# Performance work log

Hardware: AMD Instinct MI355X
Metric: run time of the kernel (lower is better)

## Reference

```python
import jax, jax.numpy as jnp
import numpy as np


def setup_inputs() -> dict:
    key = jax.random.key(0)
    ks = jax.random.split(key, 6)
    B, T, U, D, K, V = 4, 256, 64, 512, 512, 1000
    return {
        "enc_state": jax.random.normal(ks[0], (B, T, D), dtype=jnp.float32),
        "dec_state": jax.random.normal(ks[1], (B, U, D), dtype=jnp.float32),
        "W1": jax.random.normal(ks[2], (K, 2 * D), dtype=jnp.float32) * (1.0 / np.sqrt(2 * D)),
        "b1": jax.random.normal(ks[3], (K,), dtype=jnp.float32) * 0.01,
        "W2": jax.random.normal(ks[4], (V, K), dtype=jnp.float32) * (1.0 / np.sqrt(K)),
        "b2": jax.random.normal(ks[5], (V,), dtype=jnp.float32) * 0.01,
    }


def reference(enc_state, dec_state, W1, b1, W2, b2):
    # JointNet: Linear(concat(enc_bc, dec_bc)) -> tanh -> Linear.
    # Linear over the concat [enc; dec] equals split-weight matmuls broadcast-summed,
    # so we never materialize the [B,T,U,2D] concat tensor (same math).
    D_enc = enc_state.shape[-1]
    W1e, W1d = W1[:, :D_enc], W1[:, D_enc:]
    he = jnp.einsum('btd,kd->btk', enc_state, W1e)  # [B,T,K]
    hd = jnp.einsum('bud,kd->buk', dec_state, W1d)  # [B,U,K]
    h = jnp.tanh(he[:, :, None, :] + hd[:, None, :, :] + b1)  # [B,T,U,K]
    return jnp.einsum('btuk,vk->btuv', h, W2) + b2  # [B,T,U,V]
```

## Files before the change

### kernel.cpp

```cpp
#include <hip/hip_runtime.h>


typedef __bf16 bf16x8 __attribute__((ext_vector_type(8)));
typedef float  f32x4  __attribute__((ext_vector_type(4)));

#define B_   4
#define T_   256
#define U_   64
#define D_   512
#define K_   512
#define V_   1000

__device__ __forceinline__ float tanh_fast(float x) {
    float e = __expf(2.0f * x);
    float r = __builtin_amdgcn_rcpf(e + 1.0f);
    return fmaf(-2.0f, r, 1.0f);
}

__global__ __launch_bounds__(256) void w2conv_kernel(const float* __restrict__ W2,
                                                     __bf16* __restrict__ W2b) {
    int idx = (blockIdx.x * 256 + threadIdx.x) * 8;
    const f32x4* p = (const f32x4*)(W2 + idx);
    f32x4 a = p[0], b = p[1];
    bf16x8 o;
#pragma unroll
    for (int j = 0; j < 4; ++j) { o[j] = (__bf16)a[j]; o[4 + j] = (__bf16)b[j]; }
    *(bf16x8*)(W2b + idx) = o;
}

__global__ __launch_bounds__(256) void stage1_kernel(const float* __restrict__ enc,
                                                     const float* __restrict__ dec,
                                                     const float* __restrict__ W1,
                                                     float* __restrict__ he,
                                                     float* __restrict__ hd) {
    const int ct = blockIdx.x;
    const int rt = blockIdx.y;
    const bool isDec = rt >= 16;
    const float* X = isDec ? (dec + (rt - 16) * 64 * D_) : (enc + rt * 64 * D_);
    const int   woff = isDec ? D_ : 0;
    float*      Y = isDec ? (hd + (rt - 16) * 64 * K_) : (he + rt * 64 * K_);
    const int   k0 = ct * 64;

    __shared__ __align__(16) __bf16 As[64][72];
    __shared__ __align__(16) __bf16 Bs[64][72];

    const int tid  = threadIdx.x;
    const int lane = tid & 63, w = tid >> 6;
    const int wm = (w >> 1) * 32, wn = (w & 1) * 32;
    const int q = lane >> 4, li = lane & 15;

    f32x4 acc[2][2] = {};

    for (int d0 = 0; d0 < D_; d0 += 64) {
        __syncthreads();
#pragma unroll
        for (int i = 0; i < 2; ++i) {
            int s = tid + i * 256;
            int r = s >> 3, kc = s & 7;
            const f32x4* xp = (const f32x4*)(X + r * D_ + d0 + kc * 8);
            f32x4 x0 = xp[0], x1 = xp[1];
            bf16x8 a;
#pragma unroll
            for (int j = 0; j < 4; ++j) { a[j] = (__bf16)x0[j]; a[4 + j] = (__bf16)x1[j]; }
            *(bf16x8*)&As[r][kc * 8] = a;
            const f32x4* wp = (const f32x4*)(W1 + (k0 + r) * (2 * D_) + woff + d0 + kc * 8);
            f32x4 w0 = wp[0], w1 = wp[1];
            bf16x8 b;
#pragma unroll
            for (int j = 0; j < 4; ++j) { b[j] = (__bf16)w0[j]; b[4 + j] = (__bf16)w1[j]; }
            *(bf16x8*)&Bs[r][kc * 8] = b;
        }
        __syncthreads();
#pragma unroll
        for (int kk = 0; kk < 64; kk += 32) {
            bf16x8 af[2], bfr[2];
#pragma unroll
            for (int mi = 0; mi < 2; ++mi) af[mi]  = *(const bf16x8*)&As[wm + mi * 16 + li][kk + q * 8];
#pragma unroll
            for (int ni = 0; ni < 2; ++ni) bfr[ni] = *(const bf16x8*)&Bs[wn + ni * 16 + li][kk + q * 8];
#pragma unroll
            for (int mi = 0; mi < 2; ++mi)
#pragma unroll
                for (int ni = 0; ni < 2; ++ni)
                    acc[mi][ni] = __builtin_amdgcn_mfma_f32_16x16x32_bf16(af[mi], bfr[ni], acc[mi][ni], 0, 0, 0);
        }
    }
#pragma unroll
    for (int mi = 0; mi < 2; ++mi)
#pragma unroll
        for (int ni = 0; ni < 2; ++ni) {
            int row0 = wm + mi * 16 + q * 4;
            int col  = k0 + wn + ni * 16 + li;
            float* yp = Y + row0 * K_ + col;
            yp[0 * K_] = acc[mi][ni][0];
            yp[1 * K_] = acc[mi][ni][1];
            yp[2 * K_] = acc[mi][ni][2];
            yp[3 * K_] = acc[mi][ni][3];
        }
}

__global__ __launch_bounds__(256) void joint_kernel(const float* __restrict__ he,
                                                    const float* __restrict__ hd,
                                                    const float* __restrict__ b1,
                                                    const __bf16* __restrict__ W2b,
                                                    const float* __restrict__ b2,
                                                    float* __restrict__ out) {
    const int ct = blockIdx.x;
    const int rt = blockIdx.y;
    const int e0  = 2 * rt;
    const int hd0 = (rt >> 7) * 64;

    __shared__ __align__(16) __bf16 As[128][72];
    __shared__ __align__(16) __bf16 Bs[128][72];

    const int tid  = threadIdx.x;
    const int lane = tid & 63, w = tid >> 6;
    const int wm = (w >> 1) * 64, wn = (w & 1) * 64;
    const int q = lane >> 4, li = lane & 15;

    f32x4 acc[4][4] = {};

    for (int k0 = 0; k0 < K_; k0 += 64) {
        __syncthreads();
#pragma unroll
        for (int i = 0; i < 4; ++i) {
            int s = tid + i * 256;
            int m = s >> 3, kc = s & 7;
            int k = k0 + kc * 8;
            const f32x4* hp = (const f32x4*)(he + (e0 + (m >> 6)) * K_ + k);
            const f32x4* dp = (const f32x4*)(hd + (hd0 + (m & 63)) * K_ + k);
            const f32x4* bp = (const f32x4*)(b1 + k);
            f32x4 s0 = hp[0] + dp[0] + bp[0];
            f32x4 s1 = hp[1] + dp[1] + bp[1];
            bf16x8 a;
#pragma unroll
            for (int j = 0; j < 4; ++j) {
                a[j]     = (__bf16)tanh_fast(s0[j]);
                a[4 + j] = (__bf16)tanh_fast(s1[j]);
            }
            *(bf16x8*)&As[m][kc * 8] = a;
            int v = ct * 128 + m;
            bf16x8 wv;
#pragma unroll
            for (int j = 0; j < 8; ++j) wv[j] = (__bf16)0.0f;
            if (v < V_) wv = *(const bf16x8*)(W2b + v * K_ + k);
            *(bf16x8*)&Bs[m][kc * 8] = wv;
        }
        __syncthreads();
#pragma unroll
        for (int kk = 0; kk < 64; kk += 32) {
            bf16x8 af[4], bfr[4];
#pragma unroll
            for (int mi = 0; mi < 4; ++mi) af[mi]  = *(const bf16x8*)&As[wm + mi * 16 + li][kk + q * 8];
#pragma unroll
            for (int ni = 0; ni < 4; ++ni) bfr[ni] = *(const bf16x8*)&Bs[wn + ni * 16 + li][kk + q * 8];
#pragma unroll
            for (int mi = 0; mi < 4; ++mi)
#pragma unroll
                for (int ni = 0; ni < 4; ++ni)
                    acc[mi][ni] = __builtin_amdgcn_mfma_f32_16x16x32_bf16(af[mi], bfr[ni], acc[mi][ni], 0, 0, 0);
        }
    }

    const long rbase = (long)rt * 128 + wm;
#pragma unroll
    for (int ni = 0; ni < 4; ++ni) {
        int gv = ct * 128 + wn + ni * 16 + li;
        if (gv < V_) {
            float bb = b2[gv];
#pragma unroll
            for (int mi = 0; mi < 4; ++mi) {
                long r0 = rbase + mi * 16 + q * 4;
                float* op = out + r0 * V_ + gv;
                op[0 * V_] = acc[mi][ni][0] + bb;
                op[1 * V_] = acc[mi][ni][1] + bb;
                op[2 * V_] = acc[mi][ni][2] + bb;
                op[3 * V_] = acc[mi][ni][3] + bb;
            }
        }
    }
}

extern "C" void kernel_launch(void* const* d_in, const int* in_sizes, int n_in,
                              void* d_out, int out_size, void* d_ws, size_t ws_size,
                              hipStream_t stream) {
    const float* enc = (const float*)d_in[0];
    const float* dec = (const float*)d_in[1];
    const float* W1  = (const float*)d_in[2];
    const float* b1  = (const float*)d_in[3];
    const float* W2  = (const float*)d_in[4];
    const float* b2  = (const float*)d_in[5];
    float* out = (float*)d_out;

    float*  he  = (float*)d_ws;
    float*  hd  = he + 1024 * K_;
    __bf16* W2b = (__bf16*)(hd + 256 * K_);

    w2conv_kernel<<<dim3(250), dim3(256), 0, stream>>>(W2, W2b);
    stage1_kernel<<<dim3(8, 20), dim3(256), 0, stream>>>(enc, dec, W1, he, hd);
    joint_kernel<<<dim3(8, 512), dim3(256), 0, stream>>>(he, hd, b1, W2b, b2, out);
}
```

Baseline: 489.9 us.

## Materialize tanh activations in bf16 and stream GEMM tiles via direct-to-LDS loads

```diff
diff --git a/kernel.cpp b/kernel.cpp
--- a/kernel.cpp
+++ b/kernel.cpp
@@ -10,6 +10,7 @@
 #define D_   512
 #define K_   512
 #define V_   1000
+#define ROWS_ 65536L
 
 __device__ __forceinline__ float tanh_fast(float x) {
     float e = __expf(2.0f * x);
@@ -17,14 +18,27 @@
     return fmaf(-2.0f, r, 1.0f);
 }
 
+__device__ __forceinline__ void gl_lds16(const void* g, void* l) {
+    __builtin_amdgcn_global_load_lds(
+        (const __attribute__((address_space(1))) unsigned int*)g,
+        (__attribute__((address_space(3))) unsigned int*)l,
+        16, 0, 0);
+}
+
 __global__ __launch_bounds__(256) void w2conv_kernel(const float* __restrict__ W2,
                                                      __bf16* __restrict__ W2b) {
     int idx = (blockIdx.x * 256 + threadIdx.x) * 8;
-    const f32x4* p = (const f32x4*)(W2 + idx);
-    f32x4 a = p[0], b = p[1];
+    int v = idx >> 9;
     bf16x8 o;
-#pragma unroll
-    for (int j = 0; j < 4; ++j) { o[j] = (__bf16)a[j]; o[4 + j] = (__bf16)b[j]; }
+    if (v < V_) {
+        const f32x4* p = (const f32x4*)(W2 + idx);
+        f32x4 a = p[0], b = p[1];
+#pragma unroll
+        for (int j = 0; j < 4; ++j) { o[j] = (__bf16)a[j]; o[4 + j] = (__bf16)b[j]; }
+    } else {
+#pragma unroll
+        for (int j = 0; j < 8; ++j) o[j] = (__bf16)0.0f;
+    }
     *(bf16x8*)(W2b + idx) = o;
 }
 
@@ -99,61 +113,78 @@
         }
 }
 
-__global__ __launch_bounds__(256) void joint_kernel(const float* __restrict__ he,
-                                                    const float* __restrict__ hd,
-                                                    const float* __restrict__ b1,
+__global__ __launch_bounds__(256) void h_kernel(const float* __restrict__ he,
+                                                const float* __restrict__ hd,
+                                                const float* __restrict__ b1,
+                                                __bf16* __restrict__ h,
+                                                long r0) {
+    const int tid = threadIdx.x;
+    const long rl = (long)blockIdx.x * 4 + (tid >> 6);
+    const long r  = r0 + rl;
+    const int  k8 = (tid & 63) * 8;
+    const long het = r >> 6;
+    const long hdr = (r >> 14) * 64 + (r & 63);
+    const f32x4* hp = (const f32x4*)(he + het * K_ + k8);
+    const f32x4* dp = (const f32x4*)(hd + hdr * K_ + k8);
+    const f32x4* bp = (const f32x4*)(b1 + k8);
+    f32x4 s0 = hp[0] + dp[0] + bp[0];
+    f32x4 s1 = hp[1] + dp[1] + bp[1];
+    bf16x8 o;
+#pragma unroll
+    for (int j = 0; j < 4; ++j) {
+        o[j]     = (__bf16)tanh_fast(s0[j]);
+        o[4 + j] = (__bf16)tanh_fast(s1[j]);
+    }
+    *(bf16x8*)(h + rl * K_ + k8) = o;
+}
+
+__global__ __launch_bounds__(256) void joint_kernel(const __bf16* __restrict__ h,
                                                     const __bf16* __restrict__ W2b,
                                                     const float* __restrict__ b2,
-                                                    float* __restrict__ out) {
+                                                    float* __restrict__ out,
+                                                    long r0) {
     const int ct = blockIdx.x;
     const int rt = blockIdx.y;
-    const int e0  = 2 * rt;
-    const int hd0 = (rt >> 7) * 64;
-
-    __shared__ __align__(16) __bf16 As[128][72];
-    __shared__ __align__(16) __bf16 Bs[128][72];
+
+    __shared__ __align__(16) __bf16 As[128 * 64];
+    __shared__ __align__(16) __bf16 Bs[128 * 64];
 
     const int tid  = threadIdx.x;
     const int lane = tid & 63, w = tid >> 6;
     const int wm = (w >> 1) * 64, wn = (w & 1) * 64;
     const int q = lane >> 4, li = lane & 15;
 
+    const int srow = lane >> 3;
+    const int scol = ((lane & 7) ^ (srow & 7)) * 8;
+    const long aRow = (long)rt * 128 + w * 8 + srow;
+    const long bRow = (long)ct * 128 + w * 8 + srow;
+    const __bf16* aBase = h   + aRow * K_ + scol;
+    const __bf16* bBase = W2b + bRow * K_ + scol;
+    __bf16* aLds = As + w * 512;
+    __bf16* bLds = Bs + w * 512;
+
+    const int cswz0 = ((q ^ (li & 7)) * 16);
+    const char* AsB = (const char*)As;
+    const char* BsB = (const char*)Bs;
+
     f32x4 acc[4][4] = {};
 
     for (int k0 = 0; k0 < K_; k0 += 64) {
         __syncthreads();
 #pragma unroll
         for (int i = 0; i < 4; ++i) {
-            int s = tid + i * 256;
-            int m = s >> 3, kc = s & 7;
-            int k = k0 + kc * 8;
-            const f32x4* hp = (const f32x4*)(he + (e0 + (m >> 6)) * K_ + k);
-            const f32x4* dp = (const f32x4*)(hd + (hd0 + (m & 63)) * K_ + k);
-            const f32x4* bp = (const f32x4*)(b1 + k);
-            f32x4 s0 = hp[0] + dp[0] + bp[0];
-            f32x4 s1 = hp[1] + dp[1] + bp[1];
-            bf16x8 a;
-#pragma unroll
-            for (int j = 0; j < 4; ++j) {
-                a[j]     = (__bf16)tanh_fast(s0[j]);
-                a[4 + j] = (__bf16)tanh_fast(s1[j]);
-            }
-            *(bf16x8*)&As[m][kc * 8] = a;
-            int v = ct * 128 + m;
-            bf16x8 wv;
-#pragma unroll
-            for (int j = 0; j < 8; ++j) wv[j] = (__bf16)0.0f;
-            if (v < V_) wv = *(const bf16x8*)(W2b + v * K_ + k);
-            *(bf16x8*)&Bs[m][kc * 8] = wv;
-        }
-        __syncthreads();
-#pragma unroll
-        for (int kk = 0; kk < 64; kk += 32) {
+            gl_lds16(aBase + (long)i * 32 * K_ + k0, aLds + i * 2048);
+            gl_lds16(bBase + (long)i * 32 * K_ + k0, bLds + i * 2048);
+        }
+        __syncthreads();
+#pragma unroll
+        for (int kk = 0; kk < 2; ++kk) {
+            const int cs = cswz0 ^ (kk << 6);
             bf16x8 af[4], bfr[4];
 #pragma unroll
-            for (int mi = 0; mi < 4; ++mi) af[mi]  = *(const bf16x8*)&As[wm + mi * 16 + li][kk + q * 8];
-#pragma unroll
-            for (int ni = 0; ni < 4; ++ni) bfr[ni] = *(const bf16x8*)&Bs[wn + ni * 16 + li][kk + q * 8];
+            for (int mi = 0; mi < 4; ++mi) af[mi]  = *(const bf16x8*)(AsB + (wm + mi * 16 + li) * 128 + cs);
+#pragma unroll
+            for (int ni = 0; ni < 4; ++ni) bfr[ni] = *(const bf16x8*)(BsB + (wn + ni * 16 + li) * 128 + cs);
 #pragma unroll
             for (int mi = 0; mi < 4; ++mi)
 #pragma unroll
@@ -162,7 +193,7 @@
         }
     }
 
-    const long rbase = (long)rt * 128 + wm;
+    const long rbase = r0 + (long)rt * 128 + wm;
 #pragma unroll
     for (int ni = 0; ni < 4; ++ni) {
         int gv = ct * 128 + wn + ni * 16 + li;
@@ -170,12 +201,12 @@
             float bb = b2[gv];
 #pragma unroll
             for (int mi = 0; mi < 4; ++mi) {
-                long r0 = rbase + mi * 16 + q * 4;
-                float* op = out + r0 * V_ + gv;
-                op[0 * V_] = acc[mi][ni][0] + bb;
-                op[1 * V_] = acc[mi][ni][1] + bb;
-                op[2 * V_] = acc[mi][ni][2] + bb;
-                op[3 * V_] = acc[mi][ni][3] + bb;
+                long rr = rbase + mi * 16 + q * 4;
+                float* op = out + rr * V_ + gv;
+                op[0L * V_] = acc[mi][ni][0] + bb;
+                op[1L * V_] = acc[mi][ni][1] + bb;
+                op[2L * V_] = acc[mi][ni][2] + bb;
+                op[3L * V_] = acc[mi][ni][3] + bb;
             }
         }
     }
@@ -195,8 +226,19 @@
     float*  he  = (float*)d_ws;
     float*  hd  = he + 1024 * K_;
     __bf16* W2b = (__bf16*)(hd + 256 * K_);
-
-    w2conv_kernel<<<dim3(250), dim3(256), 0, stream>>>(W2, W2b);
+    __bf16* h   = W2b + 1024 * K_;
+    const size_t fixed = (size_t)(1024 + 256) * K_ * 4 + (size_t)1024 * K_ * 2;
+
+    long chunk = 0;
+    if (ws_size > fixed) chunk = (long)((ws_size - fixed) / (K_ * 2)) & ~127L;
+    if (chunk > ROWS_) chunk = ROWS_;
+    if (chunk < 128) chunk = 128;
+
+    w2conv_kernel<<<dim3(256), dim3(256), 0, stream>>>(W2, W2b);
     stage1_kernel<<<dim3(8, 20), dim3(256), 0, stream>>>(enc, dec, W1, he, hd);
-    joint_kernel<<<dim3(8, 512), dim3(256), 0, stream>>>(he, hd, b1, W2b, b2, out);
-}
+    for (long r0 = 0; r0 < ROWS_; r0 += chunk) {
+        long rows = ROWS_ - r0 < chunk ? ROWS_ - r0 : chunk;
+        h_kernel<<<dim3((int)(rows / 4)), dim3(256), 0, stream>>>(he, hd, b1, h, r0);
+        joint_kernel<<<dim3(8, (int)(rows / 128)), dim3(256), 0, stream>>>(h, W2b, b2, out, r0);
+    }
+}
```

Measured after the change: 443.6 us. 9.5% less time.
